# Optimization experiments

Measured on AMD Instinct MI355X. Metric: run time of the kernel, lower is better.

## Reference

```python
import jax, jax.numpy as jnp
import numpy as np


def _gcn_norm(edge_index, num_nodes):
    # Add self-loops (PyG SGConv default add_self_loops=True) and compute
    # symmetric normalization deg^-1/2 * A_hat * deg^-1/2.
    src, dst = edge_index[0], edge_index[1]
    loop = jnp.arange(num_nodes, dtype=src.dtype)
    src = jnp.concatenate([src, loop])
    dst = jnp.concatenate([dst, loop])
    ones = jnp.ones(src.shape[0], dtype=jnp.float32)
    deg = jax.ops.segment_sum(ones, dst, num_segments=num_nodes)
    dis = jnp.where(deg > 0, jax.lax.rsqrt(deg), 0.0)
    norm = dis[src] * dis[dst]  # per-edge weight
    return src, dst, norm


def _propagate(h, src, dst, norm, num_nodes, K):
    # K rounds of normalized sparse propagation: h <- A_hat_norm @ h
    for _ in range(K):
        h = jax.ops.segment_sum(h[src] * norm[:, None], dst, num_segments=num_nodes)
    return h


def setup_inputs() -> dict:
    key = jax.random.key(0)
    k1, k2, k3, k4 = jax.random.split(key, 4)
    N, E, F, H, C = 100000, 1600000, 128, 64, 40
    x = jax.random.normal(k1, (N, F), dtype=jnp.float32)
    edge_index = jax.random.randint(k2, (2, E), 0, N, dtype=jnp.int64)
    W1 = jax.random.normal(k3, (F, H), dtype=jnp.float32) * (1.0 / np.sqrt(F))
    b1 = jnp.zeros((H,), dtype=jnp.float32)
    W2 = jax.random.normal(k4, (H, C), dtype=jnp.float32) * (1.0 / np.sqrt(H))
    b2 = jnp.zeros((C,), dtype=jnp.float32)
    return {"x": x, "edge_index": edge_index, "W1": W1, "b1": b1, "W2": W2, "b2": b2}


def reference(x, edge_index, W1, b1, W2, b2):
    N = x.shape[0]
    K = 2
    src, dst, norm = _gcn_norm(edge_index, N)
    # SGConv layer 1: K-hop propagation then linear
    h = _propagate(x, src, dst, norm, N, K)
    h = h @ W1 + b1
    h = jax.nn.relu(h)
    # SGConv layer 2
    h = _propagate(h, src, dst, norm, N, K)
    h = h @ W2 + b2
    return jax.nn.log_softmax(h, axis=1)
```

## Files before the change

kernel.cpp:

```cpp
#include <hip/hip_runtime.h>
#include <hip/hip_fp16.h>
#include <math.h>

__host__ __device__ static inline int div_up(long long a, long long b) { return (int)((a + b - 1) / b); }

#define SCH 2048
#define PM 256
#define BKN 256
#define CAP 8192

typedef int int4v __attribute__((ext_vector_type(4)));

struct h8 { __half2 a, b, c, d; };
struct h4 { __half2 a, b; };

__device__ inline int nt_load1(const int* p) {
    return __builtin_nontemporal_load(p);
}


__global__ __launch_bounds__(256) void k_histA(const int* __restrict__ dst,
                                               int* __restrict__ histA,
                                               int E, int NBK) {
    __shared__ int h[1024];
    const int tid = threadIdx.x, c = blockIdx.x;
    for (int i = tid; i < NBK; i += 256) h[i] = 0;
    __syncthreads();
    const int ce = (div_up(E, PM) + 3) & ~3;
    const int e0 = c * ce, e1 = min(E, e0 + ce);
    int i = e0 + tid * 4;
    for (; i + 3 < e1; i += 256 * 4) {
        int4 d = *reinterpret_cast<const int4*>(dst + i);
        atomicAdd(&h[d.x >> 8], 1);
        atomicAdd(&h[d.y >> 8], 1);
        atomicAdd(&h[d.z >> 8], 1);
        atomicAdd(&h[d.w >> 8], 1);
    }
    for (int j = i; j < e1; ++j) atomicAdd(&h[dst[j] >> 8], 1);
    __syncthreads();
    for (int b = tid; b < NBK; b += 256) histA[b * PM + c] = h[b];
}

__global__ void k_scan_part(const int* __restrict__ a, int* __restrict__ bsum, int len) {
    __shared__ int ws[4];
    int base = blockIdx.x * SCH + threadIdx.x * 8;
    int t = 0;
#pragma unroll
    for (int j = 0; j < 8; ++j) {
        int idx = base + j;
        if (idx < len) t += a[idx];
    }
    for (int off = 32; off >= 1; off >>= 1) t += __shfl_xor(t, off);
    int lane = threadIdx.x & 63, wid = threadIdx.x >> 6;
    if (lane == 0) ws[wid] = t;
    __syncthreads();
    if (threadIdx.x == 0) bsum[blockIdx.x] = ws[0] + ws[1] + ws[2] + ws[3];
}

__global__ void k_scan_bsums(int* __restrict__ bsum, int* __restrict__ tot, int NB) {
    __shared__ int wsum[16];
    int tid = threadIdx.x;
    int v = (tid < NB) ? bsum[tid] : 0;
    int lane = tid & 63, wid = tid >> 6;
    int x = v;
    for (int off = 1; off < 64; off <<= 1) {
        int y = __shfl_up(x, off);
        if (lane >= off) x += y;
    }
    if (lane == 63) wsum[wid] = x;
    __syncthreads();
    if (tid < 16) {
        int s = wsum[tid];
        for (int off = 1; off < 16; off <<= 1) {
            int y = __shfl_up(s, off);
            if (tid >= off) s += y;
        }
        wsum[tid] = s;
    }
    __syncthreads();
    int woff = (wid > 0) ? wsum[wid - 1] : 0;
    int excl = woff + x - v;
    if (tid < NB) bsum[tid] = excl;
    if (tid == NB - 1) tot[0] = excl + v;
}

__global__ void k_scan_apply(const int* __restrict__ cnt, const int* __restrict__ bsum,
                             int* __restrict__ rp, int* __restrict__ cur,
                             float* __restrict__ dis, int N) {
    __shared__ int wsum[4];
    int tid = threadIdx.x;
    int base = blockIdx.x * SCH + tid * 8;
    int v[8];
    int t = 0;
#pragma unroll
    for (int j = 0; j < 8; ++j) {
        int idx = base + j;
        v[j] = (idx < N) ? cnt[idx] : 0;
        t += v[j];
    }
    int lane = tid & 63, wid = tid >> 6;
    int x = t;
    for (int off = 1; off < 64; off <<= 1) {
        int y = __shfl_up(x, off);
        if (lane >= off) x += y;
    }
    if (lane == 63) wsum[wid] = x;
    __syncthreads();
    int woff = 0;
    for (int w = 0; w < wid; ++w) woff += wsum[w];
    int run = bsum[blockIdx.x] + woff + (x - t);
#pragma unroll
    for (int j = 0; j < 8; ++j) {
        int idx = base + j;
        if (idx < N) {
            rp[idx] = run;
            cur[idx] = run;
            dis[idx] = rsqrtf((float)v[j] + 1.0f);
        }
        run += v[j];
    }
}

__global__ void k_scan_apply_plain(int* __restrict__ a, const int* __restrict__ bsum,
                                   int len) {
    __shared__ int wsum[4];
    int tid = threadIdx.x;
    int base = blockIdx.x * SCH + tid * 8;
    int v[8];
    int t = 0;
#pragma unroll
    for (int j = 0; j < 8; ++j) {
        int idx = base + j;
        v[j] = (idx < len) ? a[idx] : 0;
        t += v[j];
    }
    int lane = tid & 63, wid = tid >> 6;
    int x = t;
    for (int off = 1; off < 64; off <<= 1) {
        int y = __shfl_up(x, off);
        if (lane >= off) x += y;
    }
    if (lane == 63) wsum[wid] = x;
    __syncthreads();
    int woff = 0;
    for (int w = 0; w < wid; ++w) woff += wsum[w];
    int run = bsum[blockIdx.x] + woff + (x - t);
#pragma unroll
    for (int j = 0; j < 8; ++j) {
        int idx = base + j;
        if (idx < len) a[idx] = run;
        run += v[j];
    }
}

__global__ __launch_bounds__(256) void k_partitionA(
        const int* __restrict__ src, const int* __restrict__ dst,
        const int* __restrict__ pbase, unsigned* __restrict__ pairs, int E, int NBK) {
    __shared__ int curb[1024];
    const int tid = threadIdx.x, c = blockIdx.x;
    for (int b = tid; b < NBK; b += 256) curb[b] = pbase[b * PM + c];
    __syncthreads();
    const int ce = (div_up(E, PM) + 3) & ~3;
    const int e0 = c * ce, e1 = min(E, e0 + ce);
    int i = e0 + tid * 4;
    for (; i + 3 < e1; i += 256 * 4) {
        int4 d4 = *reinterpret_cast<const int4*>(dst + i);
        int4 s4 = *reinterpret_cast<const int4*>(src + i);
        int p0 = atomicAdd(&curb[d4.x >> 8], 1); pairs[p0] = ((unsigned)s4.x << 8) | (d4.x & 255);
        int p1 = atomicAdd(&curb[d4.y >> 8], 1); pairs[p1] = ((unsigned)s4.y << 8) | (d4.y & 255);
        int p2 = atomicAdd(&curb[d4.z >> 8], 1); pairs[p2] = ((unsigned)s4.z << 8) | (d4.z & 255);
        int p3 = atomicAdd(&curb[d4.w >> 8], 1); pairs[p3] = ((unsigned)s4.w << 8) | (d4.w & 255);
    }
    for (int j = i; j < e1; ++j) {
        int d = dst[j];
        int p = atomicAdd(&curb[d >> 8], 1);
        pairs[p] = ((unsigned)src[j] << 8) | (d & 255);
    }
}

__global__ __launch_bounds__(256) void k_cntB(
        const unsigned* __restrict__ pairs, const int* __restrict__ pbase,
        int* __restrict__ cnt, int E, int N, int NBK) {
    __shared__ int c256[BKN];
    const int b = blockIdx.x;
    const int tid = threadIdx.x;
    c256[tid] = 0;
    __syncthreads();
    const int base = pbase[b * PM];
    const int end = (b + 1 < NBK) ? pbase[(b + 1) * PM] : E;
    for (int i = base + tid; i < end; i += 256)
        atomicAdd(&c256[pairs[i] & 255], 1);
    __syncthreads();
    int n = b * BKN + tid;
    if (n < N) cnt[n] = c256[tid];
}

__global__ __launch_bounds__(256) void k_placeB(
        const unsigned* __restrict__ pairs, const int* __restrict__ rp,
        int* __restrict__ cur, int* __restrict__ csrc, int N) {
    __shared__ int curl[BKN];
    __shared__ int stage[CAP];
    const int b = blockIdx.x;
    const int n0 = b * BKN;
    const int n1 = min(N, n0 + BKN);
    const int base = rp[n0], end = rp[n1];
    const int cntb = end - base;
    const int tid = threadIdx.x;
    if (cntb <= CAP) {
        if (n0 + tid < n1) curl[tid] = rp[n0 + tid] - base;
        __syncthreads();
        for (int i = base + tid; i < end; i += 256) {
            unsigned pr = pairs[i];
            int p = atomicAdd(&curl[pr & 255], 1);
            stage[p] = (int)(pr >> 8);
        }
        __syncthreads();
        for (int i = tid; i < cntb; i += 256) csrc[base + i] = stage[i];
    } else {
        for (int i = base + tid; i < end; i += 256) {
            unsigned pr = pairs[i];
            int d = n0 + (int)(pr & 255);
            csrc[atomicAdd(&cur[d], 1)] = (int)(pr >> 8);
        }
    }
}


__device__ inline void fma_h8(float* acc, float w, const h8& v) {
    float2 f0 = __half22float2(v.a), f1 = __half22float2(v.b);
    float2 f2 = __half22float2(v.c), f3 = __half22float2(v.d);
    acc[0] += w * f0.x; acc[1] += w * f0.y;
    acc[2] += w * f1.x; acc[3] += w * f1.y;
    acc[4] += w * f2.x; acc[5] += w * f2.y;
    acc[6] += w * f3.x; acc[7] += w * f3.y;
}

template<int F>
__global__ __launch_bounds__(256) void k_prop_h(
        const int* __restrict__ rp, const int* __restrict__ csrc,
        const float* __restrict__ dis,
        const __half* __restrict__ hin, __half* __restrict__ hout, int N) {
    constexpr int TPE = F / 8;
    int t = blockIdx.x * blockDim.x + threadIdx.x;
    int n = t / TPE;
    if (n >= N) return;
    int l = t % TPE;
    float dn = dis[n];
    float acc[8];
    {
        h8 v = *reinterpret_cast<const h8*>(hin + (size_t)n * F + 8 * l);
        float wn = dn * dn;
#pragma unroll
        for (int j = 0; j < 8; ++j) acc[j] = 0.f;
        fma_h8(acc, wn, v);
    }
    int e = rp[n], end = rp[n + 1];
    for (; e + 7 < end; e += 8) {
        int s[8];
        float w[8];
        h8 v[8];
#pragma unroll
        for (int j = 0; j < 8; ++j) s[j] = nt_load1(csrc + e + j);
#pragma unroll
        for (int j = 0; j < 8; ++j) w[j] = dis[s[j]] * dn;
#pragma unroll
        for (int j = 0; j < 8; ++j)
            v[j] = *reinterpret_cast<const h8*>(hin + (size_t)s[j] * F + 8 * l);
#pragma unroll
        for (int j = 0; j < 8; ++j) fma_h8(acc, w[j], v[j]);
    }
    for (; e < end; ++e) {
        int s = nt_load1(csrc + e);
        float w = dis[s] * dn;
        h8 v = *reinterpret_cast<const h8*>(hin + (size_t)s * F + 8 * l);
        fma_h8(acc, w, v);
    }
    h8 o;
    o.a = __float22half2_rn(make_float2(acc[0], acc[1]));
    o.b = __float22half2_rn(make_float2(acc[2], acc[3]));
    o.c = __float22half2_rn(make_float2(acc[4], acc[5]));
    o.d = __float22half2_rn(make_float2(acc[6], acc[7]));
    *reinterpret_cast<h8*>(hout + (size_t)n * F + 8 * l) = o;
}


#define FMA4(a, s, v) { (a).x += (s) * (v).x; (a).y += (s) * (v).y; \
                        (a).z += (s) * (v).z; (a).w += (s) * (v).w; }

__global__ __launch_bounds__(256) void k_gemm1(const float* __restrict__ X,
                                               const float* __restrict__ W,
                                               __half* __restrict__ Y, int N) {
    __shared__ float sx[64][132];
    __shared__ float sw[128][68];
    const int tid = threadIdx.x;
    const int n0 = blockIdx.x * 64;
    const bool full = (n0 + 64 <= N);
#pragma unroll
    for (int j = 0; j < 8; ++j) {
        int idx = (tid + j * 256) * 4;
        int k = idx >> 6, h = idx & 63;
        *reinterpret_cast<float4*>(&sw[k][h]) = *reinterpret_cast<const float4*>(W + idx);
    }
#pragma unroll
    for (int j = 0; j < 8; ++j) {
        int idx = (tid + j * 256) * 4;
        int n = idx >> 7, k = idx & 127;
        float4 v = make_float4(0.f, 0.f, 0.f, 0.f);
        if (full || n0 + n < N)
            v = *reinterpret_cast<const float4*>(X + (size_t)(n0 + n) * 128 + k);
        *reinterpret_cast<float4*>(&sx[n][k]) = v;
    }
    __syncthreads();
    const int lane = tid & 63, wid = tid >> 6;
    const int h0 = (lane & 15) * 4;
    const int nb = wid * 16 + (lane >> 4) * 4;
    float4 a0 = {0,0,0,0}, a1 = {0,0,0,0}, a2 = {0,0,0,0}, a3 = {0,0,0,0};
#pragma unroll 4
    for (int k0 = 0; k0 < 128; k0 += 4) {
        float4 x0 = *reinterpret_cast<float4*>(&sx[nb + 0][k0]);
        float4 x1 = *reinterpret_cast<float4*>(&sx[nb + 1][k0]);
        float4 x2 = *reinterpret_cast<float4*>(&sx[nb + 2][k0]);
        float4 x3 = *reinterpret_cast<float4*>(&sx[nb + 3][k0]);
        float4 w0 = *reinterpret_cast<float4*>(&sw[k0 + 0][h0]);
        float4 w1 = *reinterpret_cast<float4*>(&sw[k0 + 1][h0]);
        float4 w2 = *reinterpret_cast<float4*>(&sw[k0 + 2][h0]);
        float4 w3 = *reinterpret_cast<float4*>(&sw[k0 + 3][h0]);
        FMA4(a0, x0.x, w0); FMA4(a0, x0.y, w1); FMA4(a0, x0.z, w2); FMA4(a0, x0.w, w3);
        FMA4(a1, x1.x, w0); FMA4(a1, x1.y, w1); FMA4(a1, x1.z, w2); FMA4(a1, x1.w, w3);
        FMA4(a2, x2.x, w0); FMA4(a2, x2.y, w1); FMA4(a2, x2.z, w2); FMA4(a2, x2.w, w3);
        FMA4(a3, x3.x, w0); FMA4(a3, x3.y, w1); FMA4(a3, x3.z, w2); FMA4(a3, x3.w, w3);
    }
    int n = n0 + nb;
#pragma unroll
    for (int r = 0; r < 4; ++r) {
        float4 a = (r == 0) ? a0 : (r == 1) ? a1 : (r == 2) ? a2 : a3;
        if (n + r < N) {
            h4 o;
            o.a = __float22half2_rn(make_float2(a.x, a.y));
            o.b = __float22half2_rn(make_float2(a.z, a.w));
            *reinterpret_cast<h4*>(Y + (size_t)(n + r) * 64 + h0) = o;
        }
    }
}

__global__ __launch_bounds__(256) void k_gemm2(const __half* __restrict__ H,
                                               const float* __restrict__ b1,
                                               const float* __restrict__ W2,
                                               __half* __restrict__ T, int N) {
    __shared__ float sh[64][68];
    __shared__ float sw[64][68];
    const int tid = threadIdx.x;
    const int n0 = blockIdx.x * 64;
    const bool full = (n0 + 64 <= N);
#pragma unroll
    for (int j = 0; j < 4; ++j) {
        int idx = (tid + j * 256) * 4;
        int k = idx >> 6, h = idx & 63;
        float4 v = make_float4(0.f, 0.f, 0.f, 0.f);
        if (h < 40) v = *reinterpret_cast<const float4*>(W2 + k * 40 + h);
        *reinterpret_cast<float4*>(&sw[k][h]) = v;
    }
#pragma unroll
    for (int j = 0; j < 2; ++j) {
        int idx = (tid + j * 256) * 8;
        int n = idx >> 6, k = idx & 63;
        float v[8];
        if (full || n0 + n < N) {
            h8 hv = *reinterpret_cast<const h8*>(H + (size_t)(n0 + n) * 64 + k);
            float2 f0 = __half22float2(hv.a), f1 = __half22float2(hv.b);
            float2 f2 = __half22float2(hv.c), f3 = __half22float2(hv.d);
            v[0] = f0.x; v[1] = f0.y; v[2] = f1.x; v[3] = f1.y;
            v[4] = f2.x; v[5] = f2.y; v[6] = f3.x; v[7] = f3.y;
#pragma unroll
            for (int q = 0; q < 8; ++q) v[q] = fmaxf(v[q] + b1[k + q], 0.f);
        } else {
#pragma unroll
            for (int q = 0; q < 8; ++q) v[q] = 0.f;
        }
#pragma unroll
        for (int q = 0; q < 8; ++q) sh[n][k + q] = v[q];
    }
    __syncthreads();
    const int lane = tid & 63, wid = tid >> 6;
    const int h0 = (lane & 15) * 4;
    const int nb = wid * 16 + (lane >> 4) * 4;
    float4 a0 = {0,0,0,0}, a1 = {0,0,0,0}, a2 = {0,0,0,0}, a3 = {0,0,0,0};
#pragma unroll 4
    for (int k0 = 0; k0 < 64; k0 += 4) {
        float4 x0 = *reinterpret_cast<float4*>(&sh[nb + 0][k0]);
        float4 x1 = *reinterpret_cast<float4*>(&sh[nb + 1][k0]);
        float4 x2 = *reinterpret_cast<float4*>(&sh[nb + 2][k0]);
        float4 x3 = *reinterpret_cast<float4*>(&sh[nb + 3][k0]);
        float4 w0 = *reinterpret_cast<float4*>(&sw[k0 + 0][h0]);
        float4 w1 = *reinterpret_cast<float4*>(&sw[k0 + 1][h0]);
        float4 w2 = *reinterpret_cast<float4*>(&sw[k0 + 2][h0]);
        float4 w3 = *reinterpret_cast<float4*>(&sw[k0 + 3][h0]);
        FMA4(a0, x0.x, w0); FMA4(a0, x0.y, w1); FMA4(a0, x0.z, w2); FMA4(a0, x0.w, w3);
        FMA4(a1, x1.x, w0); FMA4(a1, x1.y, w1); FMA4(a1, x1.z, w2); FMA4(a1, x1.w, w3);
        FMA4(a2, x2.x, w0); FMA4(a2, x2.y, w1); FMA4(a2, x2.z, w2); FMA4(a2, x2.w, w3);
        FMA4(a3, x3.x, w0); FMA4(a3, x3.y, w1); FMA4(a3, x3.z, w2); FMA4(a3, x3.w, w3);
    }
    if (h0 < 40) {
        int n = n0 + nb;
#pragma unroll
        for (int r = 0; r < 4; ++r) {
            float4 a = (r == 0) ? a0 : (r == 1) ? a1 : (r == 2) ? a2 : a3;
            if (n + r < N) {
                h4 o;
                o.a = __float22half2_rn(make_float2(a.x, a.y));
                o.b = __float22half2_rn(make_float2(a.z, a.w));
                *reinterpret_cast<h4*>(T + (size_t)(n + r) * 40 + h0) = o;
            }
        }
    }
}

__global__ void k_bias_lsm(const __half* __restrict__ T, const float* __restrict__ b2,
                           float* __restrict__ Y, int N) {
    int gid = blockIdx.x * blockDim.x + threadIdx.x;
    int node = gid >> 6;
    int lane = threadIdx.x & 63;
    if (node >= N) return;
    float v = (lane < 40) ? __half2float(T[(size_t)node * 40 + lane]) + b2[lane] : -INFINITY;
    float m = v;
    for (int off = 32; off >= 1; off >>= 1) m = fmaxf(m, __shfl_xor(m, off));
    float ev = (lane < 40) ? expf(v - m) : 0.0f;
    float s = ev;
    for (int off = 32; off >= 1; off >>= 1) s += __shfl_xor(s, off);
    if (lane < 40) Y[(size_t)node * 40 + lane] = v - m - logf(s);
}


extern "C" void kernel_launch(void* const* d_in, const int* in_sizes, int n_in,
                              void* d_out, int out_size, void* d_ws, size_t ws_size,
                              hipStream_t stream) {
    const float* x  = (const float*)d_in[0];
    const int*   ei = (const int*)d_in[1];
    const float* W1 = (const float*)d_in[2];
    const float* b1 = (const float*)d_in[3];
    const float* W2 = (const float*)d_in[4];
    const float* b2 = (const float*)d_in[5];
    float* out = (float*)d_out;

    const int H = in_sizes[3];
    const int F = in_sizes[2] / H;
    const int N = in_sizes[0] / F;
    const int E = in_sizes[1] / 2;
    (void)ws_size; (void)n_in; (void)out_size;

    const int* src = ei;
    const int* dst = ei + E;
    const int NSB = div_up(N, SCH);
    const int NBK = div_up(N, BKN);
    const int lenA = NBK * PM;
    const int NSA = div_up(lenA, SCH);

    const int Npad = (N + 256) & ~255;
    float* dis   = (float*)d_ws;
    int*   cnt   = (int*)(dis + Npad);
    int*   rp    = cnt + Npad;
    int*   cur   = rp + Npad;
    int*   bsum  = cur + Npad;
    int*   bsumA = bsum + 256;
    int*   histA = bsumA + 256;
    int*   csrc  = histA + ((lenA + 255) & ~255);
    __half* bufA = (__half*)(csrc + ((E + 255) & ~255));
    __half* bufB = bufA + (size_t)N * 64;
    unsigned* pairs = (unsigned*)bufB;

    const int B = 256;

    k_histA<<<PM, 256, 0, stream>>>(dst, histA, E, NBK);
    k_scan_part<<<NSA, 256, 0, stream>>>(histA, bsumA, lenA);
    k_scan_bsums<<<1, 1024, 0, stream>>>(bsumA, bsumA + 128, NSA);
    k_scan_apply_plain<<<NSA, 256, 0, stream>>>(histA, bsumA, lenA);
    k_partitionA<<<PM, 256, 0, stream>>>(src, dst, histA, pairs, E, NBK);
    k_cntB<<<NBK, 256, 0, stream>>>(pairs, histA, cnt, E, N, NBK);
    k_scan_part<<<NSB, 256, 0, stream>>>(cnt, bsum, N);
    k_scan_bsums<<<1, 1024, 0, stream>>>(bsum, rp + N, NSB);
    k_scan_apply<<<NSB, 256, 0, stream>>>(cnt, bsum, rp, cur, dis, N);
    k_placeB<<<NBK, 256, 0, stream>>>(pairs, rp, cur, csrc, N);

    k_gemm1<<<div_up(N, 64), 256, 0, stream>>>(x, W1, bufA, N);
    k_prop_h<64><<<div_up((long long)N * 8, B), B, 0, stream>>>(rp, csrc, dis, bufA, bufB, N);
    k_prop_h<64><<<div_up((long long)N * 8, B), B, 0, stream>>>(rp, csrc, dis, bufB, bufA, N);

    k_gemm2<<<div_up(N, 64), 256, 0, stream>>>(bufA, b1, W2, bufB, N);
    k_prop_h<40><<<div_up((long long)N * 5, B), B, 0, stream>>>(rp, csrc, dis, bufB, bufA, N);
    k_prop_h<40><<<div_up((long long)N * 5, B), B, 0, stream>>>(rp, csrc, dis, bufA, bufB, N);

    k_bias_lsm<<<div_up((long long)N * 64, 256), 256, 0, stream>>>(bufB, b2, out, N);
}
```

Baseline: 295.4 us.

## Fold symmetric normalization into node-side scaling and use grid-stride propagation

Rewrites the propagation so features are stored pre-scaled by deg^-1/2. Each hop then becomes a plain sum of neighbor rows times dis^2, which removes the per-edge gather of dis[src] and the per-edge multiply. The GEMMs and log-softmax apply the matching dis/inv (sqrt deg) scaling at their boundaries, and the propagation kernels switch to a fixed-size grid-stride launch. Storing pre-scaled values in half precision shifts rounding behaviour, and the fixed grid size may change load balance.

```diff
diff --git a/kernel.cpp b/kernel.cpp
--- a/kernel.cpp
+++ b/kernel.cpp
@@ -8,8 +8,7 @@
 #define PM 256
 #define BKN 256
 #define CAP 8192
-
-typedef int int4v __attribute__((ext_vector_type(4)));
+#define PROPG 2048
 
 struct h8 { __half2 a, b, c, d; };
 struct h4 { __half2 a, b; };
@@ -86,7 +85,7 @@
 
 __global__ void k_scan_apply(const int* __restrict__ cnt, const int* __restrict__ bsum,
                              int* __restrict__ rp, int* __restrict__ cur,
-                             float* __restrict__ dis, int N) {
+                             float* __restrict__ dis, float* __restrict__ inv, int N) {
     __shared__ int wsum[4];
     int tid = threadIdx.x;
     int base = blockIdx.x * SCH + tid * 8;
@@ -115,7 +114,9 @@
         if (idx < N) {
             rp[idx] = run;
             cur[idx] = run;
-            dis[idx] = rsqrtf((float)v[j] + 1.0f);
+            float dg = (float)v[j] + 1.0f;
+            dis[idx] = rsqrtf(dg);
+            inv[idx] = sqrtf(dg);
         }
         run += v[j];
     }
@@ -226,13 +227,13 @@
 }
 
 
-__device__ inline void fma_h8(float* acc, float w, const h8& v) {
+__device__ inline void add_h8(float* acc, const h8& v) {
     float2 f0 = __half22float2(v.a), f1 = __half22float2(v.b);
     float2 f2 = __half22float2(v.c), f3 = __half22float2(v.d);
-    acc[0] += w * f0.x; acc[1] += w * f0.y;
-    acc[2] += w * f1.x; acc[3] += w * f1.y;
-    acc[4] += w * f2.x; acc[5] += w * f2.y;
-    acc[6] += w * f3.x; acc[7] += w * f3.y;
+    acc[0] += f0.x; acc[1] += f0.y;
+    acc[2] += f1.x; acc[3] += f1.y;
+    acc[4] += f2.x; acc[5] += f2.y;
+    acc[6] += f3.x; acc[7] += f3.y;
 }
 
 template<int F>
@@ -241,46 +242,44 @@
         const float* __restrict__ dis,
         const __half* __restrict__ hin, __half* __restrict__ hout, int N) {
     constexpr int TPE = F / 8;
-    int t = blockIdx.x * blockDim.x + threadIdx.x;
-    int n = t / TPE;
-    if (n >= N) return;
-    int l = t % TPE;
-    float dn = dis[n];
-    float acc[8];
-    {
-        h8 v = *reinterpret_cast<const h8*>(hin + (size_t)n * F + 8 * l);
-        float wn = dn * dn;
-#pragma unroll
-        for (int j = 0; j < 8; ++j) acc[j] = 0.f;
-        fma_h8(acc, wn, v);
-    }
-    int e = rp[n], end = rp[n + 1];
-    for (; e + 7 < end; e += 8) {
-        int s[8];
-        float w[8];
-        h8 v[8];
-#pragma unroll
-        for (int j = 0; j < 8; ++j) s[j] = nt_load1(csrc + e + j);
-#pragma unroll
-        for (int j = 0; j < 8; ++j) w[j] = dis[s[j]] * dn;
-#pragma unroll
-        for (int j = 0; j < 8; ++j)
-            v[j] = *reinterpret_cast<const h8*>(hin + (size_t)s[j] * F + 8 * l);
-#pragma unroll
-        for (int j = 0; j < 8; ++j) fma_h8(acc, w[j], v[j]);
-    }
-    for (; e < end; ++e) {
-        int s = nt_load1(csrc + e);
-        float w = dis[s] * dn;
-        h8 v = *reinterpret_cast<const h8*>(hin + (size_t)s * F + 8 * l);
-        fma_h8(acc, w, v);
-    }
-    h8 o;
-    o.a = __float22half2_rn(make_float2(acc[0], acc[1]));
-    o.b = __float22half2_rn(make_float2(acc[2], acc[3]));
-    o.c = __float22half2_rn(make_float2(acc[4], acc[5]));
-    o.d = __float22half2_rn(make_float2(acc[6], acc[7]));
-    *reinterpret_cast<h8*>(hout + (size_t)n * F + 8 * l) = o;
+    const long long total = (long long)N * TPE;
+    const long long stride = (long long)gridDim.x * 256;
+    for (long long t = (long long)blockIdx.x * 256 + threadIdx.x; t < total; t += stride) {
+        int n = (int)(t / TPE);
+        int l = (int)(t % TPE);
+        float acc[8];
+        {
+            h8 v = *reinterpret_cast<const h8*>(hin + (size_t)n * F + 8 * l);
+#pragma unroll
+            for (int j = 0; j < 8; ++j) acc[j] = 0.f;
+            add_h8(acc, v);
+        }
+        int e = rp[n], end = rp[n + 1];
+        for (; e + 7 < end; e += 8) {
+            int s[8];
+            h8 v[8];
+#pragma unroll
+            for (int j = 0; j < 8; ++j) s[j] = nt_load1(csrc + e + j);
+#pragma unroll
+            for (int j = 0; j < 8; ++j)
+                v[j] = *reinterpret_cast<const h8*>(hin + (size_t)s[j] * F + 8 * l);
+#pragma unroll
+            for (int j = 0; j < 8; ++j) add_h8(acc, v[j]);
+        }
+        for (; e < end; ++e) {
+            int s = nt_load1(csrc + e);
+            h8 v = *reinterpret_cast<const h8*>(hin + (size_t)s * F + 8 * l);
+            add_h8(acc, v);
+        }
+        float dn = dis[n];
+        float d2 = dn * dn;
+        h8 o;
+        o.a = __float22half2_rn(make_float2(acc[0] * d2, acc[1] * d2));
+        o.b = __float22half2_rn(make_float2(acc[2] * d2, acc[3] * d2));
+        o.c = __float22half2_rn(make_float2(acc[4] * d2, acc[5] * d2));
+        o.d = __float22half2_rn(make_float2(acc[6] * d2, acc[7] * d2));
+        *reinterpret_cast<h8*>(hout + (size_t)n * F + 8 * l) = o;
+    }
 }
 
 
@@ -289,6 +288,7 @@
 
 __global__ __launch_bounds__(256) void k_gemm1(const float* __restrict__ X,
                                                const float* __restrict__ W,
+                                               const float* __restrict__ dis,
                                                __half* __restrict__ Y, int N) {
     __shared__ float sx[64][132];
     __shared__ float sw[128][68];
@@ -335,9 +335,10 @@
     for (int r = 0; r < 4; ++r) {
         float4 a = (r == 0) ? a0 : (r == 1) ? a1 : (r == 2) ? a2 : a3;
         if (n + r < N) {
+            float sc = dis[n + r];
             h4 o;
-            o.a = __float22half2_rn(make_float2(a.x, a.y));
-            o.b = __float22half2_rn(make_float2(a.z, a.w));
+            o.a = __float22half2_rn(make_float2(a.x * sc, a.y * sc));
+            o.b = __float22half2_rn(make_float2(a.z * sc, a.w * sc));
             *reinterpret_cast<h4*>(Y + (size_t)(n + r) * 64 + h0) = o;
         }
     }
@@ -346,6 +347,8 @@
 __global__ __launch_bounds__(256) void k_gemm2(const __half* __restrict__ H,
                                                const float* __restrict__ b1,
                                                const float* __restrict__ W2,
+                                               const float* __restrict__ dis,
+                                               const float* __restrict__ inv,
                                                __half* __restrict__ T, int N) {
     __shared__ float sh[64][68];
     __shared__ float sw[64][68];
@@ -366,13 +369,14 @@
         int n = idx >> 6, k = idx & 63;
         float v[8];
         if (full || n0 + n < N) {
+            float iv = inv[n0 + n];
             h8 hv = *reinterpret_cast<const h8*>(H + (size_t)(n0 + n) * 64 + k);
             float2 f0 = __half22float2(hv.a), f1 = __half22float2(hv.b);
             float2 f2 = __half22float2(hv.c), f3 = __half22float2(hv.d);
             v[0] = f0.x; v[1] = f0.y; v[2] = f1.x; v[3] = f1.y;
             v[4] = f2.x; v[5] = f2.y; v[6] = f3.x; v[7] = f3.y;
 #pragma unroll
-            for (int q = 0; q < 8; ++q) v[q] = fmaxf(v[q] + b1[k + q], 0.f);
+            for (int q = 0; q < 8; ++q) v[q] = fmaxf(v[q] * iv + b1[k + q], 0.f);
         } else {
 #pragma unroll
             for (int q = 0; q < 8; ++q) v[q] = 0.f;
@@ -406,9 +410,10 @@
         for (int r = 0; r < 4; ++r) {
             float4 a = (r == 0) ? a0 : (r == 1) ? a1 : (r == 2) ? a2 : a3;
             if (n + r < N) {
+                float sc = dis[n + r];
                 h4 o;
-                o.a = __float22half2_rn(make_float2(a.x, a.y));
-                o.b = __float22half2_rn(make_float2(a.z, a.w));
+                o.a = __float22half2_rn(make_float2(a.x * sc, a.y * sc));
+                o.b = __float22half2_rn(make_float2(a.z * sc, a.w * sc));
                 *reinterpret_cast<h4*>(T + (size_t)(n + r) * 40 + h0) = o;
             }
         }
@@ -416,12 +421,14 @@
 }
 
 __global__ void k_bias_lsm(const __half* __restrict__ T, const float* __restrict__ b2,
-                           float* __restrict__ Y, int N) {
+                           const float* __restrict__ inv, float* __restrict__ Y, int N) {
     int gid = blockIdx.x * blockDim.x + threadIdx.x;
     int node = gid >> 6;
     int lane = threadIdx.x & 63;
     if (node >= N) return;
-    float v = (lane < 40) ? __half2float(T[(size_t)node * 40 + lane]) + b2[lane] : -INFINITY;
+    float iv = inv[node];
+    float v = (lane < 40) ? __half2float(T[(size_t)node * 40 + lane]) * iv + b2[lane]
+                          : -INFINITY;
     float m = v;
     for (int off = 32; off >= 1; off >>= 1) m = fmaxf(m, __shfl_xor(m, off));
     float ev = (lane < 40) ? expf(v - m) : 0.0f;
@@ -457,7 +464,8 @@
 
     const int Npad = (N + 256) & ~255;
     float* dis   = (float*)d_ws;
-    int*   cnt   = (int*)(dis + Npad);
+    float* inv   = dis + Npad;
+    int*   cnt   = (int*)(inv + Npad);
     int*   rp    = cnt + Npad;
     int*   cur   = rp + Npad;
     int*   bsum  = cur + Npad;
@@ -478,16 +486,16 @@
     k_cntB<<<NBK, 256, 0, stream>>>(pairs, histA, cnt, E, N, NBK);
     k_scan_part<<<NSB, 256, 0, stream>>>(cnt, bsum, N);
     k_scan_bsums<<<1, 1024, 0, stream>>>(bsum, rp + N, NSB);
-    k_scan_apply<<<NSB, 256, 0, stream>>>(cnt, bsum, rp, cur, dis, N);
+    k_scan_apply<<<NSB, 256, 0, stream>>>(cnt, bsum, rp, cur, dis, inv, N);
     k_placeB<<<NBK, 256, 0, stream>>>(pairs, rp, cur, csrc, N);
 
-    k_gemm1<<<div_up(N, 64), 256, 0, stream>>>(x, W1, bufA, N);
-    k_prop_h<64><<<div_up((long long)N * 8, B), B, 0, stream>>>(rp, csrc, dis, bufA, bufB, N);
-    k_prop_h<64><<<div_up((long long)N * 8, B), B, 0, stream>>>(rp, csrc, dis, bufB, bufA, N);
-
-    k_gemm2<<<div_up(N, 64), 256, 0, stream>>>(bufA, b1, W2, bufB, N);
-    k_prop_h<40><<<div_up((long long)N * 5, B), B, 0, stream>>>(rp, csrc, dis, bufB, bufA, N);
-    k_prop_h<40><<<div_up((long long)N * 5, B), B, 0, stream>>>(rp, csrc, dis, bufA, bufB, N);
-
-    k_bias_lsm<<<div_up((long long)N * 64, 256), 256, 0, stream>>>(bufB, b2, out, N);
-}
+    k_gemm1<<<div_up(N, 64), 256, 0, stream>>>(x, W1, dis, bufA, N);
+    k_prop_h<64><<<PROPG, B, 0, stream>>>(rp, csrc, dis, bufA, bufB, N);
+    k_prop_h<64><<<PROPG, B, 0, stream>>>(rp, csrc, dis, bufB, bufA, N);
+
+    k_gemm2<<<div_up(N, 64), 256, 0, stream>>>(bufA, b1, W2, dis, inv, bufB, N);
+    k_prop_h<40><<<PROPG, B, 0, stream>>>(rp, csrc, dis, bufB, bufA, N);
+    k_prop_h<40><<<PROPG, B, 0, stream>>>(rp, csrc, dis, bufA, bufB, N);
+
+    k_bias_lsm<<<div_up((long long)N * 64, 256), 256, 0, stream>>>(bufB, b2, inv, out, N);
+}
```

New measurement: 281.0 us. 4.9% less time.
